# Performance work log

Hardware: AMD Instinct MI355X
Metric: run time of the kernel (lower is better)

The kernel has to match this reference:

```python
import jax, jax.numpy as jnp
import numpy as np
import math

N_USER = 50000
N_ITEM = 50000
E_PER = 400000
F_IN = 128
F_OUT = 128
H = 4
D = F_OUT // H  # 32
NUM_ET = 2  # edge types: 0 = user->item, 1 = item->user


def setup_inputs() -> dict:
    key = jax.random.key(0)
    ks = jax.random.split(key, 16)
    s = 0.05  # weight scale to keep activations tame
    return {
        "x_user": jax.random.normal(ks[0], (N_USER, F_IN), jnp.float32),
        "x_item": jax.random.normal(ks[1], (N_ITEM, F_IN), jnp.float32),
        "W_kqv_user": jax.random.normal(ks[2], (F_IN, 3 * F_OUT), jnp.float32) * s,
        "b_kqv_user": jax.random.normal(ks[3], (3 * F_OUT,), jnp.float32) * s,
        "W_kqv_item": jax.random.normal(ks[4], (F_IN, 3 * F_OUT), jnp.float32) * s,
        "b_kqv_item": jax.random.normal(ks[5], (3 * F_OUT,), jnp.float32) * s,
        "Wk_rel": jax.random.normal(ks[6], (H * NUM_ET, D, D), jnp.float32) * s,
        "Wv_rel": jax.random.normal(ks[7], (H * NUM_ET, D, D), jnp.float32) * s,
        "W_out_user": jax.random.normal(ks[8], (F_OUT, F_OUT), jnp.float32) * s,
        "b_out_user": jax.random.normal(ks[9], (F_OUT,), jnp.float32) * s,
        "W_out_item": jax.random.normal(ks[10], (F_OUT, F_OUT), jnp.float32) * s,
        "b_out_item": jax.random.normal(ks[11], (F_OUT,), jnp.float32) * s,
        "skip_user": jnp.ones((1,), jnp.float32),
        "skip_item": jnp.ones((1,), jnp.float32),
        "p_rel_ui": jnp.ones((H,), jnp.float32),
        "p_rel_iu": jnp.ones((H,), jnp.float32),
        "edge_ui": jax.random.randint(ks[12], (2, E_PER), 0, N_USER, dtype=jnp.int32),
        "edge_iu": jax.random.randint(ks[13], (2, E_PER), 0, N_ITEM, dtype=jnp.int32),
    }


def _kqv(x, W, b):
    o = x @ W + b  # [N, 3F]
    k, q, v = o[:, :F_OUT], o[:, F_OUT:2 * F_OUT], o[:, 2 * F_OUT:]
    return (k.reshape(-1, H, D), q.reshape(-1, H, D), v.reshape(-1, H, D))


def _rel(x, Wrel, et):
    # HeteroLinear with type index h*NUM_ET + et per head (is_sorted layout)
    W = Wrel[jnp.arange(H) * NUM_ET + et]  # [H, D, D]
    return jnp.einsum('nhd,hde->nhe', x, W)


def reference(x_user, x_item, W_kqv_user, b_kqv_user, W_kqv_item, b_kqv_item,
              Wk_rel, Wv_rel, W_out_user, b_out_user, W_out_item, b_out_item,
              skip_user, skip_item, p_rel_ui, p_rel_iu, edge_ui, edge_iu):
    ku, qu, vu = _kqv(x_user, W_kqv_user, b_kqv_user)
    ki, qi, vi = _kqv(x_item, W_kqv_item, b_kqv_item)

    # per-edge-type relation transform of K/V (grouped GEMM by head x edge-type)
    k0, v0 = _rel(ku, Wk_rel, 0), _rel(vu, Wv_rel, 0)  # src of user->item
    k1, v1 = _rel(ki, Wk_rel, 1), _rel(vi, Wv_rel, 1)  # src of item->user

    q_all = jnp.concatenate([qu, qi], 0)  # dst offsets: user=0, item=N_USER
    n_tot = N_USER + N_ITEM

    src0, dst0 = edge_ui[0], edge_ui[1] + N_USER
    src1, dst1 = edge_iu[0], edge_iu[1]

    kj = jnp.concatenate([k0[src0], k1[src1]], 0)  # [E, H, D]
    vj = jnp.concatenate([v0[src0], v1[src1]], 0)  # [E, H, D]
    dst = jnp.concatenate([dst0, dst1], 0)         # [E]
    p = jnp.concatenate([jnp.broadcast_to(p_rel_ui, (E_PER, H)),
                         jnp.broadcast_to(p_rel_iu, (E_PER, H))], 0)

    qe = q_all[dst]                                  # [E, H, D]
    alpha = (qe * kj).sum(-1) * p / math.sqrt(D)     # [E, H]

    # segment softmax over destination nodes (PyG softmax: max-shift, +1e-16)
    amax = jax.ops.segment_max(alpha, dst, num_segments=n_tot)
    a = jnp.exp(alpha - amax[dst])
    denom = jax.ops.segment_sum(a, dst, num_segments=n_tot)
    a = a / (denom[dst] + 1e-16)

    out = jax.ops.segment_sum(vj * a[:, :, None], dst, num_segments=n_tot)
    out = out.reshape(n_tot, F_OUT)
    out_u, out_i = out[:N_USER], out[N_USER:]

    g = lambda t: jax.nn.gelu(t, approximate=False)
    a_u = g(out_u) @ W_out_user + b_out_user
    a_i = g(out_i) @ W_out_item + b_out_item

    su = jax.nn.sigmoid(skip_user)  # out_channels == in_channels -> skip blend
    si = jax.nn.sigmoid(skip_item)
    return (su * a_u + (1.0 - su) * x_user,
            si * a_i + (1.0 - si) * x_item)
```

## Files before the change

### kernel.cpp

```cpp
#include <hip/hip_runtime.h>
#include <hip/hip_bf16.h>
#include <math.h>

#define N_USERS 50000
#define N_ITEMS 50000
#define NN      100000
#define E_PER_  400000
#define E_TOT   800000
#define FDIM    128
#define NH      4
#define HD      32
#define SCAN_CHUNK 1024
#define SCAN_NB    ((NN + SCAN_CHUNK - 1) / SCAN_CHUNK)
#define KQV_NB  ((N_USERS + 127) / 128)

typedef __attribute__((ext_vector_type(8))) short bfrag;
typedef __attribute__((ext_vector_type(4))) float f32x4;

__device__ __forceinline__ float gelu_exact(float x) {
    return 0.5f * x * (1.0f + erff(x * 0.70710678118654752f));
}
__device__ __forceinline__ unsigned short f2bf(float f) {
    unsigned u = __float_as_uint(f);
    unsigned r = u + 0x7fffu + ((u >> 16) & 1u);
    return (unsigned short)(r >> 16);
}
__device__ __forceinline__ void unpack8(uint4 u, float* f) {
    f[0] = __uint_as_float(u.x << 16); f[1] = __uint_as_float(u.x & 0xffff0000u);
    f[2] = __uint_as_float(u.y << 16); f[3] = __uint_as_float(u.y & 0xffff0000u);
    f[4] = __uint_as_float(u.z << 16); f[5] = __uint_as_float(u.z & 0xffff0000u);
    f[6] = __uint_as_float(u.w << 16); f[7] = __uint_as_float(u.w & 0xffff0000u);
}
__device__ __forceinline__ size_t wfrag_idx(int n, int k) {
    int ch = n >> 7, nt = (n >> 4) & 7, lr = n & 15;
    int ks = k >> 5, lg = (k >> 3) & 3, e = k & 7;
    return ((size_t)(((ch * 8 + nt) * 4 + ks) * 64 + lg * 16 + lr)) * 8 + e;
}

__global__ void prep_kqv(
    const float* __restrict__ W_u, const float* __restrict__ b_u,
    const float* __restrict__ W_i, const float* __restrict__ b_i,
    const float* __restrict__ Wk_rel, const float* __restrict__ Wv_rel,
    unsigned short* __restrict__ F_u, float* __restrict__ bias_u,
    unsigned short* __restrict__ F_i, float* __restrict__ bias_i)
{
    const int et = blockIdx.x >= 384;
    const int n = blockIdx.x - et * 384;
    const int k = threadIdx.x;
    const float* W = et ? W_i : W_u;
    const float* b = et ? b_i : b_u;
    unsigned short* F = et ? F_i : F_u;
    float* bias_f = et ? bias_i : bias_u;
    float s;
    if (n < 128) {
        int h = n >> 5, e = n & 31;
        const float* wr = Wk_rel + (size_t)(h * 2 + et) * 1024 + e;
        const float* wc = W + (size_t)k * 384 + h * 32;
        s = 0.f;
        for (int d = 0; d < 32; ++d) s = fmaf(wc[d], wr[d * 32], s);
        if (k == 0) {
            float bs = 0.f;
            for (int d = 0; d < 32; ++d) bs = fmaf(b[h * 32 + d], wr[d * 32], bs);
            bias_f[n] = bs;
        }
    } else if (n < 256) {
        s = W[(size_t)k * 384 + n];
        if (k == 0) bias_f[n] = b[n];
    } else {
        int h = (n - 256) >> 5, e = (n - 256) & 31;
        const float* wr = Wv_rel + (size_t)(h * 2 + et) * 1024 + e;
        const float* wc = W + (size_t)k * 384 + 256 + h * 32;
        s = 0.f;
        for (int d = 0; d < 32; ++d) s = fmaf(wc[d], wr[d * 32], s);
        if (k == 0) {
            float bs = 0.f;
            for (int d = 0; d < 32; ++d) bs = fmaf(b[256 + h * 32 + d], wr[d * 32], bs);
            bias_f[n] = bs;
        }
    }
    F[wfrag_idx(n, k)] = f2bf(s);
}

__global__ void prep_wo(
    const float* __restrict__ W_u, unsigned short* __restrict__ F_u,
    const float* __restrict__ W_i, unsigned short* __restrict__ F_i)
{
    int i = blockIdx.x * blockDim.x + threadIdx.x;
    int side = i >= 128 * 128;
    int j = i - side * 128 * 128;
    if (j >= 128 * 128) return;
    int n = j >> 7, k = j & 127;
    const float* W = side ? W_i : W_u;
    unsigned short* F = side ? F_i : F_u;
    F[wfrag_idx(n, k)] = f2bf(W[(size_t)k * 128 + n]);
}

__global__ __launch_bounds__(256, 3) void kqv_mfma(
    const float* __restrict__ X_u, const unsigned short* __restrict__ F_u,
    const float* __restrict__ bias_u,
    const float* __restrict__ X_i, const unsigned short* __restrict__ F_i,
    const float* __restrict__ bias_i,
    unsigned short* __restrict__ kk_b,
    unsigned short* __restrict__ q_b,
    unsigned short* __restrict__ vv_b)
{
    const int t = threadIdx.x;
    const int side = blockIdx.x >= KQV_NB;
    const int m0 = (blockIdx.x - side * KQV_NB) * 128;
    const float* X = side ? X_i : X_u;
    const unsigned short* F = side ? F_i : F_u;
    const float* bias = side ? bias_i : bias_u;
    const int side_off = side ? N_USERS : 0;
    const int M = N_USERS;

    const int wave = t >> 6, lane = t & 63;
    const int lr = lane & 15, lg = lane >> 4;
    const int rbase = m0 + wave * 32;

    bfrag am[2][4];
    #pragma unroll
    for (int mt = 0; mt < 2; ++mt)
        #pragma unroll
        for (int ks = 0; ks < 4; ++ks) {
            int row = rbase + mt * 16 + lr;
            float4 a = make_float4(0.f, 0.f, 0.f, 0.f);
            float4 b4 = make_float4(0.f, 0.f, 0.f, 0.f);
            if (row < M) {
                const float* px = X + (size_t)row * 128 + ks * 32 + lg * 8;
                a  = *reinterpret_cast<const float4*>(px);
                b4 = *reinterpret_cast<const float4*>(px + 4);
            }
            uint4 pk;
            pk.x = (unsigned)f2bf(a.x)  | ((unsigned)f2bf(a.y)  << 16);
            pk.y = (unsigned)f2bf(a.z)  | ((unsigned)f2bf(a.w)  << 16);
            pk.z = (unsigned)f2bf(b4.x) | ((unsigned)f2bf(b4.y) << 16);
            pk.w = (unsigned)f2bf(b4.z) | ((unsigned)f2bf(b4.w) << 16);
            am[mt][ks] = *reinterpret_cast<bfrag*>(&pk);
        }

    #pragma unroll
    for (int ch = 0; ch < 3; ++ch) {
        f32x4 acc[2][8];
        const f32x4 zero = {0.f, 0.f, 0.f, 0.f};
        #pragma unroll
        for (int mt = 0; mt < 2; ++mt)
            #pragma unroll
            for (int nt = 0; nt < 8; ++nt) acc[mt][nt] = zero;

        bfrag bc[4], bn[4];
        #pragma unroll
        for (int ks = 0; ks < 4; ++ks)
            bc[ks] = *reinterpret_cast<const bfrag*>(
                F + ((size_t)((ch * 8 + 0) * 4 + ks) * 64 + lane) * 8);

        #pragma unroll
        for (int nt = 0; nt < 8; ++nt) {
            if (nt < 7) {
                #pragma unroll
                for (int ks = 0; ks < 4; ++ks)
                    bn[ks] = *reinterpret_cast<const bfrag*>(
                        F + ((size_t)((ch * 8 + nt + 1) * 4 + ks) * 64 + lane) * 8);
            }
            #pragma unroll
            for (int mt = 0; mt < 2; ++mt)
                #pragma unroll
                for (int ks = 0; ks < 4; ++ks)
                    acc[mt][nt] = __builtin_amdgcn_mfma_f32_16x16x32_bf16(
                        bc[ks], am[mt][ks], acc[mt][nt], 0, 0, 0);
            #pragma unroll
            for (int ks = 0; ks < 4; ++ks) bc[ks] = bn[ks];
        }

        unsigned short* arr = (ch == 0) ? kk_b : (ch == 1) ? q_b : vv_b;
        #pragma unroll
        for (int nt = 0; nt < 8; ++nt) {
            float4 bv = *reinterpret_cast<const float4*>(bias + ch * 128 + nt * 16 + lg * 4);
            #pragma unroll
            for (int mt = 0; mt < 2; ++mt) {
                int row = rbase + mt * 16 + lr;
                if (row < M) {
                    unsigned lo = (unsigned)f2bf(acc[mt][nt][0] + bv.x)
                                | ((unsigned)f2bf(acc[mt][nt][1] + bv.y) << 16);
                    unsigned hi = (unsigned)f2bf(acc[mt][nt][2] + bv.z)
                                | ((unsigned)f2bf(acc[mt][nt][3] + bv.w) << 16);
                    uint2 st = make_uint2(lo, hi);
                    *reinterpret_cast<uint2*>(
                        arr + (size_t)(side_off + row) * 128 + nt * 16 + lg * 4) = st;
                }
            }
        }
    }
}

__device__ __forceinline__ void edge_src_dst(
    int e, const int* __restrict__ edge_ui, const int* __restrict__ edge_iu,
    int& src, int& dst)
{
    if (e < E_PER_) {
        src = edge_ui[e];
        dst = edge_ui[E_PER_ + e] + N_USERS;
    } else {
        int e2 = e - E_PER_;
        src = N_USERS + edge_iu[e2];
        dst = edge_iu[E_PER_ + e2];
    }
}

__global__ __launch_bounds__(256) void hist_kernel(
    const int* __restrict__ edge_ui, const int* __restrict__ edge_iu,
    int* __restrict__ cnt)
{
    int e = blockIdx.x * blockDim.x + threadIdx.x;
    if (e >= E_TOT) return;
    int src, dst;
    edge_src_dst(e, edge_ui, edge_iu, src, dst);
    atomicAdd(cnt + dst, 1);
}

__global__ __launch_bounds__(256) void scan1_kernel(
    const int* __restrict__ cnt, int* __restrict__ base, int* __restrict__ bsum)
{
    __shared__ int ssum[256];
    const int t = threadIdx.x;
    const int i0 = blockIdx.x * SCAN_CHUNK + t * 4;
    int v[4];
    #pragma unroll
    for (int j = 0; j < 4; ++j) v[j] = (i0 + j < NN) ? cnt[i0 + j] : 0;
    int tsum = v[0] + v[1] + v[2] + v[3];
    ssum[t] = tsum;
    __syncthreads();
    int run = tsum;
    for (int off = 1; off < 256; off <<= 1) {
        int o = (t >= off) ? ssum[t - off] : 0;
        __syncthreads();
        run += o;
        ssum[t] = run;
        __syncthreads();
    }
    int excl = run - tsum;
    int p = excl;
    #pragma unroll
    for (int j = 0; j < 4; ++j) {
        if (i0 + j < NN) base[i0 + j] = p;
        p += v[j];
    }
    if (t == 255) bsum[blockIdx.x] = run;
}

__global__ __launch_bounds__(256) void scan3_kernel(
    int* __restrict__ base, const int* __restrict__ bsum, int* __restrict__ cursor)
{
    const int lane = threadIdx.x & 63;
    const int chunk = blockIdx.x >> 2;
    int v0 = (lane < chunk) ? bsum[lane] : 0;
    int v1 = (64 + lane < chunk && 64 + lane < SCAN_NB) ? bsum[64 + lane] : 0;
    int s = v0 + v1;
    #pragma unroll
    for (int off = 1; off < 64; off <<= 1) s += __shfl_xor(s, off);
    int i = blockIdx.x * 256 + threadIdx.x;
    if (i < NN) {
        int b = base[i] + s;
        base[i] = b;
        cursor[i] = b;
    }
}

__global__ __launch_bounds__(256) void fill_kernel(
    const int* __restrict__ edge_ui, const int* __restrict__ edge_iu,
    int* __restrict__ cursor, int* __restrict__ esrc)
{
    int e = blockIdx.x * blockDim.x + threadIdx.x;
    if (e >= E_TOT) return;
    int src, dst;
    edge_src_dst(e, edge_ui, edge_iu, src, dst);
    int pos = atomicAdd(cursor + dst, 1);
    esrc[pos] = src;
}

__global__ __launch_bounds__(256) void attn_fused(
    const unsigned short* __restrict__ q_b, const unsigned short* __restrict__ kk_b,
    const unsigned short* __restrict__ vv_b,
    const int* __restrict__ base, const int* __restrict__ cnt,
    const int* __restrict__ esrc,
    const float* __restrict__ p_ui, const float* __restrict__ p_iu,
    unsigned short* __restrict__ oa)
{
    const int wid  = (blockIdx.x * blockDim.x + threadIdx.x) >> 6;
    const int lane = threadIdx.x & 63;
    const int nw   = (gridDim.x * blockDim.x) >> 6;
    const int g    = lane >> 4;
    const int p    = lane & 15;
    const int h    = p >> 2;
    const float rsd = 0.17677669529663687f;
    const float pu = p_ui[h], pi = p_iu[h];

    for (int n = wid; n < NN; n += nw) {
        const float pr = (n >= N_USERS) ? pu : pi;
        float qf[8];
        unpack8(*reinterpret_cast<const uint4*>(q_b + (size_t)n * 128 + p * 8), qf);
        float l = 0.f;
        float acc[8] = {0.f, 0.f, 0.f, 0.f, 0.f, 0.f, 0.f, 0.f};
        const int s0 = base[n], c = cnt[n];

        if (c > 0) {
            bool valid = g < c;
            int src = esrc[s0 + (valid ? g : 0)];
            uint4 k4 = *reinterpret_cast<const uint4*>(kk_b + (size_t)src * 128 + p * 8);
            uint4 v4 = *reinterpret_cast<const uint4*>(vv_b + (size_t)src * 128 + p * 8);

            for (int j = 0; j < c; j += 4) {
                uint4 k4n, v4n;
                bool validn = false;
                if (j + 4 < c) {
                    int jn = j + 4 + g;
                    validn = jn < c;
                    int srcn = esrc[s0 + (validn ? jn : 0)];
                    k4n = *reinterpret_cast<const uint4*>(kk_b + (size_t)srcn * 128 + p * 8);
                    v4n = *reinterpret_cast<const uint4*>(vv_b + (size_t)srcn * 128 + p * 8);
                }

                float kf[8];
                unpack8(k4, kf);
                float s = qf[0] * kf[0];
                #pragma unroll
                for (int i = 1; i < 8; ++i) s = fmaf(qf[i], kf[i], s);
                s += __shfl_xor(s, 1);
                s += __shfl_xor(s, 2);
                float w = valid ? __expf(s * pr * rsd) : 0.f;
                l += w;
                float vf[8];
                unpack8(v4, vf);
                #pragma unroll
                for (int i = 0; i < 8; ++i) acc[i] = fmaf(w, vf[i], acc[i]);

                k4 = k4n; v4 = v4n; valid = validn;
            }
        }

        l += __shfl_xor(l, 16); l += __shfl_xor(l, 32);
        #pragma unroll
        for (int i = 0; i < 8; ++i) {
            acc[i] += __shfl_xor(acc[i], 16);
            acc[i] += __shfl_xor(acc[i], 32);
        }
        if (g == 0) {
            float inv = 1.0f / (l + 1e-16f);
            uint4 pk;
            unsigned o[4];
            #pragma unroll
            for (int i = 0; i < 4; ++i) {
                o[i] = (unsigned)f2bf(acc[2 * i] * inv)
                     | ((unsigned)f2bf(acc[2 * i + 1] * inv) << 16);
            }
            pk.x = o[0]; pk.y = o[1]; pk.z = o[2]; pk.w = o[3];
            *reinterpret_cast<uint4*>(oa + (size_t)n * 128 + p * 8) = pk;
        }
    }
}

__global__ __launch_bounds__(256, 3) void final_mfma(
    const unsigned short* __restrict__ oa,
    const float* __restrict__ x_u, const unsigned short* __restrict__ F_u,
    const float* __restrict__ bo_u, const float* __restrict__ skip_u,
    const float* __restrict__ x_i, const unsigned short* __restrict__ F_i,
    const float* __restrict__ bo_i, const float* __restrict__ skip_i,
    float* __restrict__ out)
{
    const int t = threadIdx.x;
    const int side = blockIdx.x >= KQV_NB;
    const int m0 = (blockIdx.x - side * KQV_NB) * 128;
    const float* x = side ? x_i : x_u;
    const unsigned short* F = side ? F_i : F_u;
    const float* bo = side ? bo_i : bo_u;
    const float* skip = side ? skip_i : skip_u;
    const int row_off = side ? N_USERS : 0;
    const int M = N_USERS;

    const int wave = t >> 6, lane = t & 63;
    const int lr = lane & 15, lg = lane >> 4;
    const int rbase = m0 + wave * 32;

    bfrag am[2][4];
    #pragma unroll
    for (int mt = 0; mt < 2; ++mt)
        #pragma unroll
        for (int ks = 0; ks < 4; ++ks) {
            int row = rbase + mt * 16 + lr;
            uint4 u = make_uint4(0u, 0u, 0u, 0u);
            if (row < M)
                u = *reinterpret_cast<const uint4*>(
                      oa + (size_t)(row_off + row) * 128 + ks * 32 + lg * 8);
            float f[8];
            unpack8(u, f);
            #pragma unroll
            for (int e = 0; e < 8; ++e) f[e] = gelu_exact(f[e]);
            uint4 pk;
            pk.x = (unsigned)f2bf(f[0]) | ((unsigned)f2bf(f[1]) << 16);
            pk.y = (unsigned)f2bf(f[2]) | ((unsigned)f2bf(f[3]) << 16);
            pk.z = (unsigned)f2bf(f[4]) | ((unsigned)f2bf(f[5]) << 16);
            pk.w = (unsigned)f2bf(f[6]) | ((unsigned)f2bf(f[7]) << 16);
            am[mt][ks] = *reinterpret_cast<bfrag*>(&pk);
        }

    f32x4 acc[2][8];
    const f32x4 zero = {0.f, 0.f, 0.f, 0.f};
    #pragma unroll
    for (int mt = 0; mt < 2; ++mt)
        #pragma unroll
        for (int nt = 0; nt < 8; ++nt) acc[mt][nt] = zero;

    bfrag bc[4], bn[4];
    #pragma unroll
    for (int ks = 0; ks < 4; ++ks)
        bc[ks] = *reinterpret_cast<const bfrag*>(
            F + ((size_t)(0 * 4 + ks) * 64 + lane) * 8);

    #pragma unroll
    for (int nt = 0; nt < 8; ++nt) {
        if (nt < 7) {
            #pragma unroll
            for (int ks = 0; ks < 4; ++ks)
                bn[ks] = *reinterpret_cast<const bfrag*>(
                    F + ((size_t)((nt + 1) * 4 + ks) * 64 + lane) * 8);
        }
        #pragma unroll
        for (int mt = 0; mt < 2; ++mt)
            #pragma unroll
            for (int ks = 0; ks < 4; ++ks)
                acc[mt][nt] = __builtin_amdgcn_mfma_f32_16x16x32_bf16(
                    bc[ks], am[mt][ks], acc[mt][nt], 0, 0, 0);
        #pragma unroll
        for (int ks = 0; ks < 4; ++ks) bc[ks] = bn[ks];
    }

    const float sg = 1.0f / (1.0f + expf(-skip[0]));
    #pragma unroll
    for (int nt = 0; nt < 8; ++nt) {
        float4 bv = *reinterpret_cast<const float4*>(bo + nt * 16 + lg * 4);
        #pragma unroll
        for (int mt = 0; mt < 2; ++mt) {
            int row = rbase + mt * 16 + lr;
            if (row < M) {
                float4 xv = *reinterpret_cast<const float4*>(
                    x + (size_t)row * 128 + nt * 16 + lg * 4);
                float4 res;
                res.x = sg * (acc[mt][nt][0] + bv.x) + (1.f - sg) * xv.x;
                res.y = sg * (acc[mt][nt][1] + bv.y) + (1.f - sg) * xv.y;
                res.z = sg * (acc[mt][nt][2] + bv.z) + (1.f - sg) * xv.z;
                res.w = sg * (acc[mt][nt][3] + bv.w) + (1.f - sg) * xv.w;
                *reinterpret_cast<float4*>(
                    out + (size_t)(row_off + row) * 128 + nt * 16 + lg * 4) = res;
            }
        }
    }
}

extern "C" void kernel_launch(void* const* d_in, const int* in_sizes, int n_in,
                              void* d_out, int out_size, void* d_ws, size_t ws_size,
                              hipStream_t stream)
{
    const float* x_user     = (const float*)d_in[0];
    const float* x_item     = (const float*)d_in[1];
    const float* W_kqv_user = (const float*)d_in[2];
    const float* b_kqv_user = (const float*)d_in[3];
    const float* W_kqv_item = (const float*)d_in[4];
    const float* b_kqv_item = (const float*)d_in[5];
    const float* Wk_rel     = (const float*)d_in[6];
    const float* Wv_rel     = (const float*)d_in[7];
    const float* W_out_user = (const float*)d_in[8];
    const float* b_out_user = (const float*)d_in[9];
    const float* W_out_item = (const float*)d_in[10];
    const float* b_out_item = (const float*)d_in[11];
    const float* skip_user  = (const float*)d_in[12];
    const float* skip_item  = (const float*)d_in[13];
    const float* p_ui       = (const float*)d_in[14];
    const float* p_iu       = (const float*)d_in[15];
    const int*   edge_ui    = (const int*)d_in[16];
    const int*   edge_iu    = (const int*)d_in[17];

    const size_t NODE_F = (size_t)NN * FDIM;
    char* w = (char*)d_ws;
    size_t off = 0;
    auto alloc = [&](size_t bytes) {
        char* p = w + off;
        off += (bytes + 255) & ~(size_t)255;
        return p;
    };
    unsigned short* q_b   = (unsigned short*)alloc(NODE_F * 2);
    unsigned short* kk_b  = (unsigned short*)alloc(NODE_F * 2);
    unsigned short* vv_b  = (unsigned short*)alloc(NODE_F * 2);
    unsigned short* oa_b  = (unsigned short*)alloc(NODE_F * 2);
    int* esrc   = (int*)alloc((size_t)E_TOT * 4);
    int* cnt    = (int*)alloc((size_t)NN * 4);
    int* base   = (int*)alloc((size_t)NN * 4);
    int* cursor = (int*)alloc((size_t)NN * 4);
    int* bsum   = (int*)alloc((size_t)SCAN_NB * 4);
    unsigned short* F_u    = (unsigned short*)alloc(384 * 128 * 2);
    unsigned short* F_i    = (unsigned short*)alloc(384 * 128 * 2);
    float*          bias_u = (float*)alloc(384 * 4);
    float*          bias_i = (float*)alloc(384 * 4);
    unsigned short* Fo_u   = (unsigned short*)alloc(128 * 128 * 2);
    unsigned short* Fo_i   = (unsigned short*)alloc(128 * 128 * 2);

    prep_kqv<<<768, 128, 0, stream>>>(W_kqv_user, b_kqv_user, W_kqv_item, b_kqv_item,
                                      Wk_rel, Wv_rel, F_u, bias_u, F_i, bias_i);
    prep_wo<<<128, 256, 0, stream>>>(W_out_user, Fo_u, W_out_item, Fo_i);

    kqv_mfma<<<2 * KQV_NB, 256, 0, stream>>>(x_user, F_u, bias_u,
                                             x_item, F_i, bias_i,
                                             kk_b, q_b, vv_b);

    hipMemsetAsync(cnt, 0, (size_t)NN * 4, stream);
    hist_kernel<<<(E_TOT + 255) / 256, 256, 0, stream>>>(edge_ui, edge_iu, cnt);
    scan1_kernel<<<SCAN_NB, 256, 0, stream>>>(cnt, base, bsum);
    scan3_kernel<<<(NN + 255) / 256, 256, 0, stream>>>(base, bsum, cursor);
    fill_kernel<<<(E_TOT + 255) / 256, 256, 0, stream>>>(edge_ui, edge_iu, cursor, esrc);

    attn_fused<<<2048, 256, 0, stream>>>(q_b, kk_b, vv_b, base, cnt, esrc,
                                         p_ui, p_iu, oa_b);

    final_mfma<<<2 * KQV_NB, 256, 0, stream>>>(
        oa_b, x_user, Fo_u, b_out_user, skip_user,
        x_item, Fo_i, b_out_item, skip_item, (float*)d_out);
}
```

Before: 257.2 us.

## Process 8 edges per wave in attention and move GELU into attention epilogue

The attention kernel now maps 8 lanes per edge, each holding 16 features, so a wave handles 8 edges per iteration instead of 4. The old software prefetch of the next edge's K/V is removed. The final reduction becomes a butterfly reduce-scatter, so every lane writes 2 outputs. GELU is applied in that epilogue before the bf16 store, and the final GEMM now loads pre-activated fragments directly instead of recomputing GELU per tile. Wider loads per lane add memory parallelism, at the cost of more registers and losing the explicit prefetch overlap.

```diff
diff --git a/kernel.cpp b/kernel.cpp
--- a/kernel.cpp
+++ b/kernel.cpp
@@ -288,73 +288,80 @@
     const int wid  = (blockIdx.x * blockDim.x + threadIdx.x) >> 6;
     const int lane = threadIdx.x & 63;
     const int nw   = (gridDim.x * blockDim.x) >> 6;
-    const int g    = lane >> 4;
-    const int p    = lane & 15;
-    const int h    = p >> 2;
+    const int g    = lane >> 3;
+    const int p    = lane & 7;
+    const int h    = p >> 1;
     const float rsd = 0.17677669529663687f;
     const float pu = p_ui[h], pi = p_iu[h];
 
     for (int n = wid; n < NN; n += nw) {
         const float pr = (n >= N_USERS) ? pu : pi;
-        float qf[8];
-        unpack8(*reinterpret_cast<const uint4*>(q_b + (size_t)n * 128 + p * 8), qf);
+        float qf[16];
+        {
+            const unsigned short* qrow = q_b + (size_t)n * 128 + p * 16;
+            unpack8(*reinterpret_cast<const uint4*>(qrow), qf);
+            unpack8(*reinterpret_cast<const uint4*>(qrow + 8), qf + 8);
+        }
         float l = 0.f;
-        float acc[8] = {0.f, 0.f, 0.f, 0.f, 0.f, 0.f, 0.f, 0.f};
+        float acc[16];
+        #pragma unroll
+        for (int i = 0; i < 16; ++i) acc[i] = 0.f;
         const int s0 = base[n], c = cnt[n];
 
-        if (c > 0) {
-            bool valid = g < c;
-            int src = esrc[s0 + (valid ? g : 0)];
-            uint4 k4 = *reinterpret_cast<const uint4*>(kk_b + (size_t)src * 128 + p * 8);
-            uint4 v4 = *reinterpret_cast<const uint4*>(vv_b + (size_t)src * 128 + p * 8);
-
-            for (int j = 0; j < c; j += 4) {
-                uint4 k4n, v4n;
-                bool validn = false;
-                if (j + 4 < c) {
-                    int jn = j + 4 + g;
-                    validn = jn < c;
-                    int srcn = esrc[s0 + (validn ? jn : 0)];
-                    k4n = *reinterpret_cast<const uint4*>(kk_b + (size_t)srcn * 128 + p * 8);
-                    v4n = *reinterpret_cast<const uint4*>(vv_b + (size_t)srcn * 128 + p * 8);
-                }
-
-                float kf[8];
-                unpack8(k4, kf);
-                float s = qf[0] * kf[0];
-                #pragma unroll
-                for (int i = 1; i < 8; ++i) s = fmaf(qf[i], kf[i], s);
-                s += __shfl_xor(s, 1);
-                s += __shfl_xor(s, 2);
-                float w = valid ? __expf(s * pr * rsd) : 0.f;
-                l += w;
-                float vf[8];
-                unpack8(v4, vf);
-                #pragma unroll
-                for (int i = 0; i < 8; ++i) acc[i] = fmaf(w, vf[i], acc[i]);
-
-                k4 = k4n; v4 = v4n; valid = validn;
-            }
-        }
-
-        l += __shfl_xor(l, 16); l += __shfl_xor(l, 32);
+        for (int j = 0; j < c; j += 8) {
+            int jj = j + g;
+            bool valid = jj < c;
+            int src = esrc[s0 + (valid ? jj : 0)];
+            const unsigned short* krow = kk_b + (size_t)src * 128 + p * 16;
+            const unsigned short* vrow = vv_b + (size_t)src * 128 + p * 16;
+            uint4 k4a = *reinterpret_cast<const uint4*>(krow);
+            uint4 k4b = *reinterpret_cast<const uint4*>(krow + 8);
+            uint4 v4a = *reinterpret_cast<const uint4*>(vrow);
+            uint4 v4b = *reinterpret_cast<const uint4*>(vrow + 8);
+            float kf[16];
+            unpack8(k4a, kf); unpack8(k4b, kf + 8);
+            float s = qf[0] * kf[0];
+            #pragma unroll
+            for (int i = 1; i < 16; ++i) s = fmaf(qf[i], kf[i], s);
+            s += __shfl_xor(s, 1);
+            float w = valid ? __expf(s * pr * rsd) : 0.f;
+            l += w;
+            float vf[16];
+            unpack8(v4a, vf); unpack8(v4b, vf + 8);
+            #pragma unroll
+            for (int i = 0; i < 16; ++i) acc[i] = fmaf(w, vf[i], acc[i]);
+        }
+
+        l += __shfl_xor(l, 8); l += __shfl_xor(l, 16); l += __shfl_xor(l, 32);
+
+        const bool b2 = (g & 4) != 0;
+        float k8[8];
         #pragma unroll
         for (int i = 0; i < 8; ++i) {
-            acc[i] += __shfl_xor(acc[i], 16);
-            acc[i] += __shfl_xor(acc[i], 32);
-        }
-        if (g == 0) {
-            float inv = 1.0f / (l + 1e-16f);
-            uint4 pk;
-            unsigned o[4];
-            #pragma unroll
-            for (int i = 0; i < 4; ++i) {
-                o[i] = (unsigned)f2bf(acc[2 * i] * inv)
-                     | ((unsigned)f2bf(acc[2 * i + 1] * inv) << 16);
-            }
-            pk.x = o[0]; pk.y = o[1]; pk.z = o[2]; pk.w = o[3];
-            *reinterpret_cast<uint4*>(oa + (size_t)n * 128 + p * 8) = pk;
-        }
+            float mine = b2 ? acc[8 + i] : acc[i];
+            float send = b2 ? acc[i] : acc[8 + i];
+            k8[i] = mine + __shfl_xor(send, 32);
+        }
+        const bool b1 = (g & 2) != 0;
+        float k4r[4];
+        #pragma unroll
+        for (int i = 0; i < 4; ++i) {
+            float mine = b1 ? k8[4 + i] : k8[i];
+            float send = b1 ? k8[i] : k8[4 + i];
+            k4r[i] = mine + __shfl_xor(send, 16);
+        }
+        const bool b0 = (g & 1) != 0;
+        float k2[2];
+        #pragma unroll
+        for (int i = 0; i < 2; ++i) {
+            float mine = b0 ? k4r[2 + i] : k4r[i];
+            float send = b0 ? k4r[i] : k4r[2 + i];
+            k2[i] = mine + __shfl_xor(send, 8);
+        }
+        float inv = 1.0f / (l + 1e-16f);
+        unsigned pk = (unsigned)f2bf(gelu_exact(k2[0] * inv))
+                    | ((unsigned)f2bf(gelu_exact(k2[1] * inv)) << 16);
+        *reinterpret_cast<unsigned*>(oa + (size_t)n * 128 + p * 16 + 2 * g) = pk;
     }
 }
 
@@ -381,25 +388,16 @@
     const int rbase = m0 + wave * 32;
 
     bfrag am[2][4];
+    const bfrag bz = {0, 0, 0, 0, 0, 0, 0, 0};
     #pragma unroll
     for (int mt = 0; mt < 2; ++mt)
         #pragma unroll
         for (int ks = 0; ks < 4; ++ks) {
             int row = rbase + mt * 16 + lr;
-            uint4 u = make_uint4(0u, 0u, 0u, 0u);
-            if (row < M)
-                u = *reinterpret_cast<const uint4*>(
-                      oa + (size_t)(row_off + row) * 128 + ks * 32 + lg * 8);
-            float f[8];
-            unpack8(u, f);
-            #pragma unroll
-            for (int e = 0; e < 8; ++e) f[e] = gelu_exact(f[e]);
-            uint4 pk;
-            pk.x = (unsigned)f2bf(f[0]) | ((unsigned)f2bf(f[1]) << 16);
-            pk.y = (unsigned)f2bf(f[2]) | ((unsigned)f2bf(f[3]) << 16);
-            pk.z = (unsigned)f2bf(f[4]) | ((unsigned)f2bf(f[5]) << 16);
-            pk.w = (unsigned)f2bf(f[6]) | ((unsigned)f2bf(f[7]) << 16);
-            am[mt][ks] = *reinterpret_cast<bfrag*>(&pk);
+            am[mt][ks] = (row < M)
+                ? *reinterpret_cast<const bfrag*>(
+                      oa + (size_t)(row_off + row) * 128 + ks * 32 + lg * 8)
+                : bz;
         }
 
     f32x4 acc[2][8];
```

Result: faster. 244.6 us (-4.9%).

## Fuse GELU into attention epilogue, use reduce-scatter shuffles, pack base/count metadata

Applied to the files above, without the earlier changes.

The attention kernel now reduces its per-group accumulators with a reduce-scatter shuffle pattern instead of a full all-reduce. Each of the four lane groups ends up owning two of the eight outputs, so every lane applies GELU and writes one packed bf16 pair. GELU moves out of the final MFMA kernel's operand load, which now reads the activated bf16 values directly as fragments. Segment base and count are packed into one int2 array written by the scan kernel, so each node needs a single 8-byte metadata load. The cost is an extra NN*8 buffer write in the scan stage and narrower 4-byte stores from attention.

```diff
diff --git a/kernel.cpp b/kernel.cpp
--- a/kernel.cpp
+++ b/kernel.cpp
@@ -248,7 +248,9 @@
 }
 
 __global__ __launch_bounds__(256) void scan3_kernel(
-    int* __restrict__ base, const int* __restrict__ bsum, int* __restrict__ cursor)
+    const int* __restrict__ base, const int* __restrict__ bsum,
+    const int* __restrict__ cnt,
+    int* __restrict__ cursor, int2* __restrict__ meta2)
 {
     const int lane = threadIdx.x & 63;
     const int chunk = blockIdx.x >> 2;
@@ -260,8 +262,8 @@
     int i = blockIdx.x * 256 + threadIdx.x;
     if (i < NN) {
         int b = base[i] + s;
-        base[i] = b;
         cursor[i] = b;
+        meta2[i] = make_int2(b, cnt[i]);
     }
 }
 
@@ -280,8 +282,7 @@
 __global__ __launch_bounds__(256) void attn_fused(
     const unsigned short* __restrict__ q_b, const unsigned short* __restrict__ kk_b,
     const unsigned short* __restrict__ vv_b,
-    const int* __restrict__ base, const int* __restrict__ cnt,
-    const int* __restrict__ esrc,
+    const int2* __restrict__ meta2, const int* __restrict__ esrc,
     const float* __restrict__ p_ui, const float* __restrict__ p_iu,
     unsigned short* __restrict__ oa)
 {
@@ -300,7 +301,8 @@
         unpack8(*reinterpret_cast<const uint4*>(q_b + (size_t)n * 128 + p * 8), qf);
         float l = 0.f;
         float acc[8] = {0.f, 0.f, 0.f, 0.f, 0.f, 0.f, 0.f, 0.f};
-        const int s0 = base[n], c = cnt[n];
+        const int2 mt = meta2[n];
+        const int s0 = mt.x, c = mt.y;
 
         if (c > 0) {
             bool valid = g < c;
@@ -338,23 +340,27 @@
         }
 
         l += __shfl_xor(l, 16); l += __shfl_xor(l, 32);
-        #pragma unroll
-        for (int i = 0; i < 8; ++i) {
-            acc[i] += __shfl_xor(acc[i], 16);
-            acc[i] += __shfl_xor(acc[i], 32);
-        }
-        if (g == 0) {
-            float inv = 1.0f / (l + 1e-16f);
-            uint4 pk;
-            unsigned o[4];
-            #pragma unroll
-            for (int i = 0; i < 4; ++i) {
-                o[i] = (unsigned)f2bf(acc[2 * i] * inv)
-                     | ((unsigned)f2bf(acc[2 * i + 1] * inv) << 16);
-            }
-            pk.x = o[0]; pk.y = o[1]; pk.z = o[2]; pk.w = o[3];
-            *reinterpret_cast<uint4*>(oa + (size_t)n * 128 + p * 8) = pk;
-        }
+
+        const bool b1 = (g & 2) != 0;
+        float k4r[4];
+        #pragma unroll
+        for (int i = 0; i < 4; ++i) {
+            float mine = b1 ? acc[4 + i] : acc[i];
+            float send = b1 ? acc[i] : acc[4 + i];
+            k4r[i] = mine + __shfl_xor(send, 32);
+        }
+        const bool b0 = (g & 1) != 0;
+        float k2[2];
+        #pragma unroll
+        for (int i = 0; i < 2; ++i) {
+            float mine = b0 ? k4r[2 + i] : k4r[i];
+            float send = b0 ? k4r[i] : k4r[2 + i];
+            k2[i] = mine + __shfl_xor(send, 16);
+        }
+        float inv = 1.0f / (l + 1e-16f);
+        unsigned pk = (unsigned)f2bf(gelu_exact(k2[0] * inv))
+                    | ((unsigned)f2bf(gelu_exact(k2[1] * inv)) << 16);
+        *reinterpret_cast<unsigned*>(oa + (size_t)n * 128 + p * 8 + 2 * g) = pk;
     }
 }
 
@@ -381,25 +387,16 @@
     const int rbase = m0 + wave * 32;
 
     bfrag am[2][4];
+    const bfrag bz = {0, 0, 0, 0, 0, 0, 0, 0};
     #pragma unroll
     for (int mt = 0; mt < 2; ++mt)
         #pragma unroll
         for (int ks = 0; ks < 4; ++ks) {
             int row = rbase + mt * 16 + lr;
-            uint4 u = make_uint4(0u, 0u, 0u, 0u);
-            if (row < M)
-                u = *reinterpret_cast<const uint4*>(
-                      oa + (size_t)(row_off + row) * 128 + ks * 32 + lg * 8);
-            float f[8];
-            unpack8(u, f);
-            #pragma unroll
-            for (int e = 0; e < 8; ++e) f[e] = gelu_exact(f[e]);
-            uint4 pk;
-            pk.x = (unsigned)f2bf(f[0]) | ((unsigned)f2bf(f[1]) << 16);
-            pk.y = (unsigned)f2bf(f[2]) | ((unsigned)f2bf(f[3]) << 16);
-            pk.z = (unsigned)f2bf(f[4]) | ((unsigned)f2bf(f[5]) << 16);
-            pk.w = (unsigned)f2bf(f[6]) | ((unsigned)f2bf(f[7]) << 16);
-            am[mt][ks] = *reinterpret_cast<bfrag*>(&pk);
+            am[mt][ks] = (row < M)
+                ? *reinterpret_cast<const bfrag*>(
+                      oa + (size_t)(row_off + row) * 128 + ks * 32 + lg * 8)
+                : bz;
         }
 
     f32x4 acc[2][8];
@@ -495,6 +492,7 @@
     int* base   = (int*)alloc((size_t)NN * 4);
     int* cursor = (int*)alloc((size_t)NN * 4);
     int* bsum   = (int*)alloc((size_t)SCAN_NB * 4);
+    int2* meta2 = (int2*)alloc((size_t)NN * 8);
     unsigned short* F_u    = (unsigned short*)alloc(384 * 128 * 2);
     unsigned short* F_i    = (unsigned short*)alloc(384 * 128 * 2);
     float*          bias_u = (float*)alloc(384 * 4);
@@ -513,10 +511,10 @@
     hipMemsetAsync(cnt, 0, (size_t)NN * 4, stream);
     hist_kernel<<<(E_TOT + 255) / 256, 256, 0, stream>>>(edge_ui, edge_iu, cnt);
     scan1_kernel<<<SCAN_NB, 256, 0, stream>>>(cnt, base, bsum);
-    scan3_kernel<<<(NN + 255) / 256, 256, 0, stream>>>(base, bsum, cursor);
+    scan3_kernel<<<(NN + 255) / 256, 256, 0, stream>>>(base, bsum, cnt, cursor, meta2);
     fill_kernel<<<(E_TOT + 255) / 256, 256, 0, stream>>>(edge_ui, edge_iu, cursor, esrc);
 
-    attn_fused<<<2048, 256, 0, stream>>>(q_b, kk_b, vv_b, base, cnt, esrc,
+    attn_fused<<<2048, 256, 0, stream>>>(q_b, kk_b, vv_b, meta2, esrc,
                                          p_ui, p_iu, oa_b);
 
     final_mfma<<<2 * KQV_NB, 256, 0, stream>>>(
```

Measured after the change: 242.1 us. 1.06x faster.
